# Performance work log

Measured on AMD Instinct MI355X. Metric: run time of the kernel, lower is better.

The kernel has to match this reference:

```python
import jax, jax.numpy as jnp
import numpy as np

MAX_WORDS = 128  # static word capacity (stands in for dynamic max_word_num)


def setup_inputs() -> dict:
    key = jax.random.key(0)
    k1, k2 = jax.random.split(key)
    L, B, D = 512, 256, 256
    char_feats = jax.random.normal(k1, (L, B, D), dtype=jnp.float32)
    # sorted random word ids, densified so each row's ids are contiguous 0..n-1
    raw = jnp.sort(jax.random.randint(k2, (B, L), 0, MAX_WORDS), axis=1)
    bump = jnp.concatenate(
        [jnp.zeros((B, 1), jnp.int32), (raw[:, 1:] != raw[:, :-1]).astype(jnp.int32)],
        axis=1,
    )
    word_ids = jnp.cumsum(bump, axis=1)  # [B, L], non-decreasing, < MAX_WORDS
    attention_mask = jnp.ones((B, L), dtype=jnp.int32)
    return {"char_feats": char_feats, "word_ids": word_ids, "attention_mask": attention_mask}


def _pool(char_feats, word_ids, attention_mask):
    # char_feats: [L, B, D] time-major; word_ids/attention_mask: [B, L]
    L, B, D = char_feats.shape
    char_nums = jnp.sum(attention_mask, axis=1) - 2  # drop [CLS]/[SEP]
    pos = jnp.arange(L)
    # chars at positions 1 .. char_nums (inclusive) participate, per torch slicing
    valid = (pos[None, :] >= 1) & (pos[None, :] < 1 + char_nums[:, None])  # [B, L]
    seg = jnp.where(valid, word_ids, MAX_WORDS)  # overflow bucket for invalid chars
    feats_bld = jnp.transpose(char_feats, (1, 0, 2))  # [B, L, D]

    seg_sum = jax.vmap(
        lambda s, f: jax.ops.segment_sum(f, s, num_segments=MAX_WORDS + 1)
    )(seg, feats_bld)[:, :MAX_WORDS]  # [B, W, D]
    counts = jax.vmap(
        lambda s: jax.ops.segment_sum(jnp.ones((L,), jnp.float32), s, num_segments=MAX_WORDS + 1)
    )(seg)[:, :MAX_WORDS]  # [B, W]

    word_nums = jnp.max(word_ids, axis=1) + 1  # [B]
    masks = jnp.arange(MAX_WORDS)[:, None] < word_nums[None, :]  # [W, B]
    means = seg_sum / jnp.maximum(counts, 1.0)[..., None]  # counts>=1 within word_num
    word_feats = jnp.where(masks.T[..., None], means, 0.0)  # zero padded word slots
    return jnp.transpose(word_feats, (1, 0, 2)), masks  # [W, B, D], [W, B]


def reference(char_feats, word_ids, attention_mask):
    return _pool(char_feats, word_ids, attention_mask)
```

## Files before the change

kernel.cpp:

```cpp
#include <hip/hip_runtime.h>
#include <hip/hip_bf16.h>

#define LSEQ 512
#define BATCH 256
#define DIM 256
#define WMAX 128
#define ROW4 (BATCH * DIM / 4)
#define BD4 (DIM / 4)
#define MSTRIDE (WMAX + 2)

__global__ __launch_bounds__(256) void meta_kernel(
    const int* __restrict__ word_ids,
    const int* __restrict__ amask,
    int* __restrict__ meta,
    float* __restrict__ out)
{
    const int b = blockIdx.x;
    const int t = threadIdx.x;
    const int lane = t & 63;
    const int wi = t >> 6;

    __shared__ int sids[LSEQ];
    __shared__ int spart[4];
    __shared__ int sstart[WMAX + 1];

    int msum = 0;
    if (t < 128) {
        ((int4*)sids)[t] = ((const int4*)(word_ids + b * LSEQ))[t];
    } else {
        int4 m = ((const int4*)(amask + b * LSEQ))[t - 128];
        msum = m.x + m.y + m.z + m.w;
    }
    #pragma unroll
    for (int off = 32; off; off >>= 1) msum += __shfl_down(msum, off, 64);
    if (lane == 0) spart[wi] = msum;
    __syncthreads();

    const int char_num = spart[0] + spart[1] + spart[2] + spart[3] - 2;
    int pend = 1 + char_num;
    if (pend < 1) pend = 1;
    if (pend > LSEQ) pend = LSEQ;

    if (t <= WMAX) sstart[t] = pend;
    __syncthreads();

    for (int p = 1 + t; p < pend; p += 256) {
        if (p == 1 || sids[p] != sids[p - 1]) sstart[sids[p]] = p;
    }
    if (t == 0) sstart[0] = 1;
    __syncthreads();

    if (t <= WMAX) meta[b * MSTRIDE + t] = sstart[t];

    if (t < WMAX) {
        int word_num = sids[LSEQ - 1] + 1;
        out[(size_t)WMAX * BATCH * DIM + (size_t)t * BATCH + b] =
            (t < word_num) ? 1.0f : 0.0f;
    }
}

__global__ __launch_bounds__(256) void pool_kernel(
    const float* __restrict__ feats,
    const int* __restrict__ meta,
    float* __restrict__ out)
{
    const int b = blockIdx.x & (BATCH - 1);
    const int wg = blockIdx.x >> 8;
    const int t = threadIdx.x;
    const int lane = t & 63;
    const int w = wg * 4 + (t >> 6);

    const int* m = meta + b * MSTRIDE;
    const int s0 = m[w];
    const int s1 = m[w + 1];
    const int c = s1 - s0;

    const float4* __restrict__ f4 = (const float4*)feats;
    const int boff = b * BD4 + lane;

    float4 acc = make_float4(0.f, 0.f, 0.f, 0.f);
    for (int i = 0; i < c; i += 8) {
        const int n = c - i;
        float4 v[8];
        #pragma unroll
        for (int j = 0; j < 8; j++) {
            if (j < n) v[j] = f4[(size_t)(s0 + i + j) * ROW4 + boff];
        }
        #pragma unroll
        for (int j = 0; j < 8; j++) {
            if (j < n) {
                acc.x += v[j].x; acc.y += v[j].y;
                acc.z += v[j].z; acc.w += v[j].w;
            }
        }
    }

    const float inv = 1.0f / (float)(c > 0 ? c : 1);
    ((float4*)out)[(size_t)w * ROW4 + boff] =
        make_float4(acc.x * inv, acc.y * inv, acc.z * inv, acc.w * inv);
}

extern "C" void kernel_launch(void* const* d_in, const int* in_sizes, int n_in,
                              void* d_out, int out_size, void* d_ws, size_t ws_size,
                              hipStream_t stream) {
    const float* char_feats = (const float*)d_in[0];
    const int* word_ids     = (const int*)d_in[1];
    const int* amask        = (const int*)d_in[2];
    float* out              = (float*)d_out;
    int* meta               = (int*)d_ws;

    meta_kernel<<<BATCH, 256, 0, stream>>>(word_ids, amask, meta, out);
    pool_kernel<<<BATCH * 32, 256, 0, stream>>>(char_feats, meta, out);
}
```

Measured before the change: 203.5 us.

## Pool eight consecutive words per wavefront with double-buffered streaming row loads

Each wavefront now handles a span of eight consecutive words instead of one. It streams the rows of the span with double-buffered 8-row register prefetch and writes each word's mean when its boundary is crossed. The aim is to keep more loads in flight per wavefront, to cut per-word launch overhead, and to avoid the load stalls at the end of short words. In exchange the grid shrinks eightfold, to 1024 blocks, which could reduce parallelism and balance across CUs when word lengths vary.

```diff
diff --git a/kernel.cpp b/kernel.cpp
--- a/kernel.cpp
+++ b/kernel.cpp
@@ -8,6 +8,7 @@
 #define ROW4 (BATCH * DIM / 4)
 #define BD4 (DIM / 4)
 #define MSTRIDE (WMAX + 2)
+#define WPW 8
 
 __global__ __launch_bounds__(256) void meta_kernel(
     const int* __restrict__ word_ids,
@@ -59,45 +60,80 @@
     }
 }
 
-__global__ __launch_bounds__(256) void pool_kernel(
+__global__ __launch_bounds__(256, 4) void pool_kernel(
     const float* __restrict__ feats,
     const int* __restrict__ meta,
     float* __restrict__ out)
 {
     const int b = blockIdx.x & (BATCH - 1);
-    const int wg = blockIdx.x >> 8;
+    const int wcg = blockIdx.x >> 8;
     const int t = threadIdx.x;
     const int lane = t & 63;
-    const int w = wg * 4 + (t >> 6);
+    const int wi = t >> 6;
+    const int w0 = (wcg * 4 + wi) * WPW;
 
-    const int* m = meta + b * MSTRIDE;
-    const int s0 = m[w];
-    const int s1 = m[w + 1];
-    const int c = s1 - s0;
+    const int* mb = meta + __builtin_amdgcn_readfirstlane(b * MSTRIDE + w0);
+    int bnd[WPW + 1];
+    #pragma unroll
+    for (int i = 0; i <= WPW; i++) bnd[i] = mb[i];
 
     const float4* __restrict__ f4 = (const float4*)feats;
+    float4* __restrict__ o4 = (float4*)out;
     const int boff = b * BD4 + lane;
 
+    const int R0 = bnd[0];
+    const int R1 = bnd[WPW];
+
     float4 acc = make_float4(0.f, 0.f, 0.f, 0.f);
-    for (int i = 0; i < c; i += 8) {
-        const int n = c - i;
-        float4 v[8];
+    int cur = 0;
+    int nxt = bnd[1];
+
+    if (R0 < R1) {
+        int p = R0;
+        float4 A[8], Bv[8];
         #pragma unroll
         for (int j = 0; j < 8; j++) {
-            if (j < n) v[j] = f4[(size_t)(s0 + i + j) * ROW4 + boff];
+            int r = p + j;
+            A[j] = f4[(size_t)(r < R1 ? r : R1 - 1) * ROW4 + boff];
         }
-        #pragma unroll
-        for (int j = 0; j < 8; j++) {
-            if (j < n) {
-                acc.x += v[j].x; acc.y += v[j].y;
-                acc.z += v[j].z; acc.w += v[j].w;
+        while (p < R1) {
+            #pragma unroll
+            for (int j = 0; j < 8; j++) {
+                int r = p + 8 + j;
+                Bv[j] = f4[(size_t)(r < R1 ? r : R1 - 1) * ROW4 + boff];
             }
+            int n = R1 - p; if (n > 8) n = 8;
+            #pragma unroll
+            for (int j = 0; j < 8; j++) {
+                if (j < n) {
+                    const int pp = p + j;
+                    while (pp >= nxt) {
+                        const int c = nxt - bnd[cur];
+                        const float inv = 1.0f / (float)(c > 0 ? c : 1);
+                        o4[(size_t)(w0 + cur) * ROW4 + boff] = make_float4(
+                            acc.x * inv, acc.y * inv, acc.z * inv, acc.w * inv);
+                        acc = make_float4(0.f, 0.f, 0.f, 0.f);
+                        cur++;
+                        nxt = bnd[cur + 1];
+                    }
+                    acc.x += A[j].x; acc.y += A[j].y;
+                    acc.z += A[j].z; acc.w += A[j].w;
+                }
+            }
+            #pragma unroll
+            for (int j = 0; j < 8; j++) A[j] = Bv[j];
+            p += 8;
         }
     }
 
-    const float inv = 1.0f / (float)(c > 0 ? c : 1);
-    ((float4*)out)[(size_t)w * ROW4 + boff] =
-        make_float4(acc.x * inv, acc.y * inv, acc.z * inv, acc.w * inv);
+    while (cur < WPW) {
+        const int c = bnd[cur + 1] - bnd[cur];
+        const float inv = 1.0f / (float)(c > 0 ? c : 1);
+        o4[(size_t)(w0 + cur) * ROW4 + boff] = make_float4(
+            acc.x * inv, acc.y * inv, acc.z * inv, acc.w * inv);
+        acc = make_float4(0.f, 0.f, 0.f, 0.f);
+        cur++;
+    }
 }
 
 extern "C" void kernel_launch(void* const* d_in, const int* in_sizes, int n_in,
@@ -110,5 +146,5 @@
     int* meta               = (int*)d_ws;
 
     meta_kernel<<<BATCH, 256, 0, stream>>>(word_ids, amask, meta, out);
-    pool_kernel<<<BATCH * 32, 256, 0, stream>>>(char_feats, meta, out);
+    pool_kernel<<<BATCH * 4, 256, 0, stream>>>(char_feats, meta, out);
 }
```

Result: no change. 206.5 us (+1.5%).
